# Performance work log

Measured on AMD Instinct MI355X. Metric: run time of the kernel, lower is better.

Reference implementation:

```python
import jax, jax.numpy as jnp
import numpy as np

B = 16384  # batch
D = 1024   # input_size (== hidden_size, required by the original code)
H = 1024   # hidden_size


def setup_inputs() -> dict:
    key = jax.random.key(0)
    ks = jax.random.split(key, 20)
    s = 0.02
    inp = {
        "x": jax.random.normal(ks[0], (B, D), dtype=jnp.float32),
        "h": jax.random.normal(ks[1], (B, H), dtype=jnp.float32),
        "c_prev": jax.random.normal(ks[2], (B, H), dtype=jnp.float32),
    }
    names = ["i_x", "f_x", "c_x", "o_x", "i_h", "f_h", "c_h", "o_h"]
    for n, name in enumerate(names):
        in_dim = D if name.endswith("_x") else H
        inp["W" + name] = jax.random.normal(ks[3 + 2 * n], (H, in_dim), dtype=jnp.float32) * s
        inp["b" + name] = jax.random.normal(ks[4 + 2 * n], (H,), dtype=jnp.float32) * s
    return inp


def reference(x, h, c_prev,
              Wi_x, bi_x, Wf_x, bf_x, Wc_x, bc_x, Wo_x, bo_x,
              Wi_h, bi_h, Wf_h, bf_h, Wc_h, bc_h, Wo_h, bo_h):
    # NOTE: the original module applies NO sigmoid to the gates; i, f, o are raw affine sums.
    i = x @ Wi_x.T + bi_x + h @ Wi_h.T + bi_h
    f = x @ Wf_x.T + bf_x + h @ Wf_h.T + bf_h
    g = jnp.tanh(x @ Wc_x.T + bc_x + h @ Wc_h.T + bc_h)
    o = x @ Wo_x.T + bo_x + h @ Wo_h.T + bo_h
    c_next = g * i + c_prev * f
    h_next = o * jnp.tanh(c_next)
    return (h_next, c_next)
```

## Files before the change

### kernel.cpp

```cpp
#include <hip/hip_runtime.h>
#include <hip/hip_bf16.h>


#define MROWS 16384
#define NCOLS 1024
#define KTOT  2048

typedef __attribute__((ext_vector_type(8))) short bf16x8;
typedef __attribute__((ext_vector_type(4))) float f32x4;
typedef unsigned int u32;
typedef unsigned short u16;

__device__ __forceinline__ u16 f2bf(float f) {
  union { float f; u32 u; } v; v.f = f;
  u32 r = v.u + 0x7fffu + ((v.u >> 16) & 1u);
  return (u16)(r >> 16);
}

__device__ __forceinline__ bf16x8 pack8(float4 lo, float4 hi) {
  bf16x8 v;
  v[0] = (short)f2bf(lo.x); v[1] = (short)f2bf(lo.y);
  v[2] = (short)f2bf(lo.z); v[3] = (short)f2bf(lo.w);
  v[4] = (short)f2bf(hi.x); v[5] = (short)f2bf(hi.y);
  v[6] = (short)f2bf(hi.z); v[7] = (short)f2bf(hi.w);
  return v;
}

__device__ __forceinline__ float tanh_fast(float x) {
  float e = __expf(2.0f * x);
  return 1.0f - 2.0f / (e + 1.0f);
}

typedef __attribute__((address_space(1))) const u32 gas_u32;
typedef __attribute__((address_space(3))) u32 las_u32;

__device__ __forceinline__ void gl_lds16(const void* g, void* l) {
  __builtin_amdgcn_global_load_lds((gas_u32*)g, (las_u32*)l, 16, 0, 0);
}

__global__ void __launch_bounds__(256) convA(const float* __restrict__ x,
                                             const float* __restrict__ h,
                                             u16* __restrict__ A) {
  u32 t = blockIdx.x * 256u + threadIdx.x;
  #pragma unroll
  for (int i = 0; i < 4; ++i) {
    u32 chunk = t + (u32)i * 1048576u;
    u32 row = chunk >> 8;
    u32 cpos = (chunk & 255u) * 8u;
    const float* src = (cpos < 1024u) ? (x + (size_t)row * 1024 + cpos)
                                      : (h + (size_t)row * 1024 + (cpos - 1024u));
    float4 lo = *(const float4*)src;
    float4 hi = *(const float4*)(src + 4);
    *(bf16x8*)(A + (size_t)chunk * 8) = pack8(lo, hi);
  }
}

__global__ void __launch_bounds__(256) convW(const float* __restrict__ wix, const float* __restrict__ wfx,
                                             const float* __restrict__ wcx, const float* __restrict__ wox,
                                             const float* __restrict__ wih, const float* __restrict__ wfh,
                                             const float* __restrict__ wch, const float* __restrict__ woh,
                                             u16* __restrict__ W) {
  u32 t = blockIdx.x * 256u + threadIdx.x;
  const float* WX[4] = {wix, wfx, wcx, wox};
  const float* WH[4] = {wih, wfh, wch, woh};
  #pragma unroll
  for (int g = 0; g < 4; ++g) {
    u32 c3 = t;
    u32 n = c3 >> 8;
    u32 cpos = (c3 & 255u) * 8u;
    const float* src = (cpos < 1024u) ? (WX[g] + (size_t)n * 1024 + cpos)
                                      : (WH[g] + (size_t)n * 1024 + (cpos - 1024u));
    float4 lo = *(const float4*)src;
    float4 hi = *(const float4*)(src + 4);
    *(bf16x8*)(W + (size_t)g * 2097152 + (size_t)c3 * 8) = pack8(lo, hi);
  }
}

__global__ void __launch_bounds__(512) lstm_gemm2(
    const u16* __restrict__ Abf, const u16* __restrict__ Wbf,
    const float* __restrict__ bix, const float* __restrict__ bfx,
    const float* __restrict__ bcx, const float* __restrict__ box_,
    const float* __restrict__ bih, const float* __restrict__ bfh,
    const float* __restrict__ bch, const float* __restrict__ boh,
    const float* __restrict__ cprev, float* __restrict__ out) {
  __shared__ alignas(16) u16 sA[2 * 16384];
  __shared__ alignas(16) u16 sB[2 * 16384];

  const u32 tid = threadIdx.x;
  const u32 lane = tid & 63u, wid = tid >> 6;
  const u32 wr = wid >> 1, wc = wid & 1u;
  const u32 l15 = lane & 15u, l4 = lane >> 4;

  const u32 bid = blockIdx.x;
  const u32 sid = (bid & 7u) * 128u + (bid >> 3);
  const u32 bm = sid >> 4, bn = sid & 15u;

  const u16* gAp[4];
  const u16* gBp[4];
  #pragma unroll
  for (int j = 0; j < 4; ++j) {
    u32 chunk = wid * 256u + (u32)j * 64u + lane;
    u32 row = chunk >> 3, k8 = chunk & 7u;
    u32 col16 = k8 ^ (row & 7u);
    gAp[j] = Abf + (size_t)(bm * 256u + row) * KTOT + col16 * 8u;
    u32 Wrow = (row >> 6) * 1024u + bn * 64u + (row & 63u);
    gBp[j] = Wbf + (size_t)Wrow * KTOT + col16 * 8u;
  }

#define STAGE(ktile, dbuf) do { \
    _Pragma("unroll") \
    for (int j = 0; j < 4; ++j) { \
      u32 dst = (dbuf) * 16384u + (wid * 256u + (u32)j * 64u) * 8u; \
      gl_lds16(gAp[j] + (u32)(ktile) * 64u, sA + dst); \
      gl_lds16(gBp[j] + (u32)(ktile) * 64u, sB + dst); \
    } \
  } while (0)

  const char* cA = (const char*)sA;
  const char* cB = (const char*)sB;
  const u32 kb[2] = { l4 * 16u, 64u + l4 * 16u };

  f32x4 acc[4][4][2];
  #pragma unroll
  for (int mf = 0; mf < 4; ++mf)
    #pragma unroll
    for (int g = 0; g < 4; ++g)
      #pragma unroll
      for (int nf = 0; nf < 2; ++nf)
        acc[mf][g][nf] = (f32x4){0.f, 0.f, 0.f, 0.f};

  STAGE(0, 0);
  __syncthreads();

  #pragma unroll 2
  for (int kt = 0; kt < 32; ++kt) {
    const u32 d = (u32)kt & 1u, dn = d ^ 1u;
    const u32 dO = d * 32768u;

    if (kt < 31) STAGE(kt + 1, dn);
    __builtin_amdgcn_sched_barrier(0);

    bf16x8 af[4][2];
    #pragma unroll
    for (int mf = 0; mf < 4; ++mf) {
      u32 mrow = wr * 64u + (u32)mf * 16u + l15;
      u32 rb = dO + mrow * 128u;
      u32 sw = (mrow & 7u) << 4;
      af[mf][0] = *(const bf16x8*)(cA + rb + (kb[0] ^ sw));
      af[mf][1] = *(const bf16x8*)(cA + rb + (kb[1] ^ sw));
    }

    __builtin_amdgcn_s_setprio(1);
    #pragma unroll
    for (int s = 0; s < 2; ++s)
      #pragma unroll
      for (int g = 0; g < 4; ++g)
        #pragma unroll
        for (int nf = 0; nf < 2; ++nf) {
          u32 brow = (u32)g * 64u + wc * 32u + (u32)nf * 16u + l15;
          u32 off = dO + brow * 128u + (kb[s] ^ ((brow & 7u) << 4));
          bf16x8 bfr = *(const bf16x8*)(cB + off);
          #pragma unroll
          for (int mf = 0; mf < 4; ++mf)
            acc[mf][g][nf] = __builtin_amdgcn_mfma_f32_16x16x32_bf16(af[mf][s], bfr, acc[mf][g][nf], 0, 0, 0);
        }
    __builtin_amdgcn_s_setprio(0);

    __syncthreads();
  }
#undef STAGE

  #pragma unroll
  for (int nf = 0; nf < 2; ++nf) {
    u32 col = bn * 64u + wc * 32u + (u32)nf * 16u + l15;
    float bi = bix[col] + bih[col];
    float bff = bfx[col] + bfh[col];
    float bc = bcx[col] + bch[col];
    float bo = box_[col] + boh[col];
    #pragma unroll
    for (int mf = 0; mf < 4; ++mf) {
      u32 row0 = bm * 256u + wr * 64u + (u32)mf * 16u + l4 * 4u;
      #pragma unroll
      for (int r = 0; r < 4; ++r) {
        size_t idx = (size_t)(row0 + (u32)r) * 1024 + col;
        float iv = acc[mf][0][nf][r] + bi;
        float fv = acc[mf][1][nf][r] + bff;
        float gv = tanh_fast(acc[mf][2][nf][r] + bc);
        float ov = acc[mf][3][nf][r] + bo;
        float cp = cprev[idx];
        float cn = gv * iv + cp * fv;
        out[idx] = ov * tanh_fast(cn);
        out[(size_t)16777216 + idx] = cn;
      }
    }
  }
}

__global__ void __launch_bounds__(256, 2) lstm_gemm_fb(
    const float* __restrict__ x, const float* __restrict__ h,
    const float* __restrict__ wix, const float* __restrict__ wfx,
    const float* __restrict__ wcx, const float* __restrict__ wox,
    const float* __restrict__ wih, const float* __restrict__ wfh,
    const float* __restrict__ wch, const float* __restrict__ woh,
    const float* __restrict__ bix, const float* __restrict__ bfx,
    const float* __restrict__ bcx, const float* __restrict__ box_,
    const float* __restrict__ bih, const float* __restrict__ bfh,
    const float* __restrict__ bch, const float* __restrict__ boh,
    const float* __restrict__ cprev, float* __restrict__ out) {
  __shared__ alignas(16) u16 sA[128 * 64];
  __shared__ alignas(16) u16 sB[4 * 64 * 64];
  const u32 tid = threadIdx.x;
  const u32 lane = tid & 63u;
  const u32 wid = tid >> 6;
  const u32 wr = wid >> 1, wc = wid & 1u;
  const u32 bidx = blockIdx.x;
  const u32 bm = bidx >> 4, bn = bidx & 15u;
  f32x4 acc[4][4][2];
  #pragma unroll
  for (int g = 0; g < 4; ++g)
    #pragma unroll
    for (int m = 0; m < 4; ++m)
      #pragma unroll
      for (int n = 0; n < 2; ++n)
        acc[g][m][n] = (f32x4){0.f, 0.f, 0.f, 0.f};
  const u32 l15 = lane & 15u, l4 = lane >> 4;
  for (int kt = 0; kt < KTOT / 64; ++kt) {
    const u32 k0 = (u32)kt * 64u;
    if (kt) __syncthreads();
    #pragma unroll
    for (int c = 0; c < 4; ++c) {
      u32 chunk = tid + (u32)c * 256u;
      u32 row = chunk >> 3;
      u32 cp = (chunk & 7u) * 8u;
      u32 gk = k0 + cp;
      const float* src = (gk < 1024u) ? (x + (size_t)(bm * 128u + row) * 1024 + gk)
                                      : (h + (size_t)(bm * 128u + row) * 1024 + (gk - 1024u));
      float4 lo = *(const float4*)src;
      float4 hi = *(const float4*)(src + 4);
      u32 dst = row * 128u + ((cp * 2u) ^ ((row & 7u) << 4));
      *(bf16x8*)((char*)sA + dst) = pack8(lo, hi);
    }
    #pragma unroll
    for (int g = 0; g < 4; ++g) {
      const float* Wxg = (g == 0) ? wix : (g == 1) ? wfx : (g == 2) ? wcx : wox;
      const float* Whg = (g == 0) ? wih : (g == 1) ? wfh : (g == 2) ? wch : woh;
      #pragma unroll
      for (int cc = 0; cc < 2; ++cc) {
        u32 c3 = tid + (u32)cc * 256u;
        u32 row = c3 >> 3;
        u32 cp = (c3 & 7u) * 8u;
        u32 gk = k0 + cp;
        const float* src = (gk < 1024u) ? (Wxg + (size_t)(bn * 64u + row) * 1024 + gk)
                                        : (Whg + (size_t)(bn * 64u + row) * 1024 + (gk - 1024u));
        float4 lo = *(const float4*)src;
        float4 hi = *(const float4*)(src + 4);
        u32 dst = (u32)g * 8192u + row * 128u + ((cp * 2u) ^ ((row & 7u) << 4));
        *(bf16x8*)((char*)sB + dst) = pack8(lo, hi);
      }
    }
    __syncthreads();
    #pragma unroll
    for (int s = 0; s < 2; ++s) {
      bf16x8 af[4];
      #pragma unroll
      for (int m = 0; m < 4; ++m) {
        u32 mrow = wr * 64u + (u32)m * 16u + l15;
        u32 off = mrow * 128u + (((u32)s * 64u + l4 * 16u) ^ ((mrow & 7u) << 4));
        af[m] = *(const bf16x8*)((const char*)sA + off);
      }
      #pragma unroll
      for (int g = 0; g < 4; ++g) {
        #pragma unroll
        for (int nf = 0; nf < 2; ++nf) {
          u32 nrow = wc * 32u + (u32)nf * 16u + l15;
          u32 off = (u32)g * 8192u + nrow * 128u +
                    (((u32)s * 64u + l4 * 16u) ^ ((nrow & 7u) << 4));
          bf16x8 bfr = *(const bf16x8*)((const char*)sB + off);
          #pragma unroll
          for (int m = 0; m < 4; ++m)
            acc[g][m][nf] = __builtin_amdgcn_mfma_f32_16x16x32_bf16(af[m], bfr, acc[g][m][nf], 0, 0, 0);
        }
      }
    }
  }
  #pragma unroll
  for (int nf = 0; nf < 2; ++nf) {
    u32 col = bn * 64u + wc * 32u + (u32)nf * 16u + l15;
    float bi = bix[col] + bih[col];
    float bff = bfx[col] + bfh[col];
    float bc = bcx[col] + bch[col];
    float bo = box_[col] + boh[col];
    #pragma unroll
    for (int m = 0; m < 4; ++m) {
      u32 row0 = bm * 128u + wr * 64u + (u32)m * 16u + l4 * 4u;
      #pragma unroll
      for (int r = 0; r < 4; ++r) {
        size_t idx = (size_t)(row0 + (u32)r) * 1024 + col;
        float iv = acc[0][m][nf][r] + bi;
        float fv = acc[1][m][nf][r] + bff;
        float gv = tanh_fast(acc[2][m][nf][r] + bc);
        float ov = acc[3][m][nf][r] + bo;
        float cp = cprev[idx];
        float cn = gv * iv + cp * fv;
        out[idx] = ov * tanh_fast(cn);
        out[(size_t)16777216 + idx] = cn;
      }
    }
  }
}

extern "C" void kernel_launch(void* const* d_in, const int* in_sizes, int n_in,
                              void* d_out, int out_size, void* d_ws, size_t ws_size,
                              hipStream_t stream) {
  const float* x = (const float*)d_in[0];
  const float* h = (const float*)d_in[1];
  const float* cprev = (const float*)d_in[2];
  const float* wix = (const float*)d_in[3];  const float* bix = (const float*)d_in[4];
  const float* wfx = (const float*)d_in[5];  const float* bfx = (const float*)d_in[6];
  const float* wcx = (const float*)d_in[7];  const float* bcx = (const float*)d_in[8];
  const float* wox = (const float*)d_in[9];  const float* box_ = (const float*)d_in[10];
  const float* wih = (const float*)d_in[11]; const float* bih = (const float*)d_in[12];
  const float* wfh = (const float*)d_in[13]; const float* bfh = (const float*)d_in[14];
  const float* wch = (const float*)d_in[15]; const float* bch = (const float*)d_in[16];
  const float* woh = (const float*)d_in[17]; const float* boh = (const float*)d_in[18];
  float* out = (float*)d_out;

  const size_t needA = (size_t)MROWS * KTOT * 2;
  const size_t needW = (size_t)4 * NCOLS * KTOT * 2;

  if (ws_size >= needA + needW) {
    u16* Abf = (u16*)d_ws;
    u16* Wbf = (u16*)((char*)d_ws + needA);
    convA<<<dim3(4096), dim3(256), 0, stream>>>(x, h, Abf);
    convW<<<dim3(1024), dim3(256), 0, stream>>>(wix, wfx, wcx, wox, wih, wfh, wch, woh, Wbf);
    lstm_gemm2<<<dim3(1024), dim3(512), 0, stream>>>(
        Abf, Wbf, bix, bfx, bcx, box_, bih, bfh, bch, boh, cprev, out);
  } else {
    lstm_gemm_fb<<<dim3(2048), dim3(256), 0, stream>>>(
        x, h, wix, wfx, wcx, wox, wih, wfh, wch, woh,
        bix, bfx, bcx, box_, bih, bfh, bch, boh, cprev, out);
  }
}
```

Measured before the change: 357.2 us.

## Shrink GEMM block tile to 128x256 with K-tile 32 for two blocks per CU

Replaces the 512-thread, 256x256-output block with 256-thread blocks covering 128 rows by 256 gate-columns, and halves the K tile from 64 to 32. LDS use per block falls from 128KB to 48KB, so two blocks can be resident per CU and the grid doubles to 2048 blocks. The swizzle is adapted to 4 chunks per row, and the XCD block remapping is adjusted for the larger grid. In exchange, the smaller tile lowers operand reuse, so more LDS and global traffic is needed per FLOP, and there are twice as many K iterations, each with its own barrier.

```diff
diff --git a/kernel.cpp b/kernel.cpp
--- a/kernel.cpp
+++ b/kernel.cpp
@@ -76,94 +76,92 @@
   }
 }
 
-__global__ void __launch_bounds__(512) lstm_gemm2(
+__global__ void __launch_bounds__(256, 2) lstm_gemm3(
     const u16* __restrict__ Abf, const u16* __restrict__ Wbf,
     const float* __restrict__ bix, const float* __restrict__ bfx,
     const float* __restrict__ bcx, const float* __restrict__ box_,
     const float* __restrict__ bih, const float* __restrict__ bfh,
     const float* __restrict__ bch, const float* __restrict__ boh,
     const float* __restrict__ cprev, float* __restrict__ out) {
-  __shared__ alignas(16) u16 sA[2 * 16384];
-  __shared__ alignas(16) u16 sB[2 * 16384];
+  __shared__ alignas(16) u16 sA[2 * 4096];
+  __shared__ alignas(16) u16 sB[2 * 8192];
 
   const u32 tid = threadIdx.x;
-  const u32 lane = tid & 63u, wid = tid >> 6;
+  const u32 lane = tid & 63u;
+  const u32 wid = tid >> 6;
   const u32 wr = wid >> 1, wc = wid & 1u;
   const u32 l15 = lane & 15u, l4 = lane >> 4;
 
-  const u32 bid = blockIdx.x;
-  const u32 sid = (bid & 7u) * 128u + (bid >> 3);
+  const u32 bidx = blockIdx.x;
+  const u32 sid = (bidx & 7u) * 256u + (bidx >> 3);
   const u32 bm = sid >> 4, bn = sid & 15u;
 
-  const u16* gAp[4];
+  const u16* gAp[2];
   const u16* gBp[4];
   #pragma unroll
+  for (int j = 0; j < 2; ++j) {
+    u32 c = (wid * 2u + (u32)j) * 64u + lane;
+    u32 row = c >> 2, k8 = c & 3u;
+    u32 col16 = k8 ^ (row & 3u);
+    gAp[j] = Abf + (size_t)(bm * 128u + row) * KTOT + col16 * 8u;
+  }
+  #pragma unroll
   for (int j = 0; j < 4; ++j) {
-    u32 chunk = wid * 256u + (u32)j * 64u + lane;
-    u32 row = chunk >> 3, k8 = chunk & 7u;
-    u32 col16 = k8 ^ (row & 7u);
-    gAp[j] = Abf + (size_t)(bm * 256u + row) * KTOT + col16 * 8u;
-    u32 Wrow = (row >> 6) * 1024u + bn * 64u + (row & 63u);
-    gBp[j] = Wbf + (size_t)Wrow * KTOT + col16 * 8u;
+    u32 c = (wid * 4u + (u32)j) * 64u + lane;
+    u32 brow = c >> 2, k8 = c & 3u;
+    u32 Wrow = (brow >> 6) * 1024u + bn * 64u + (brow & 63u);
+    gBp[j] = Wbf + (size_t)Wrow * KTOT + (k8 ^ (brow & 3u)) * 8u;
   }
 
 #define STAGE(ktile, dbuf) do { \
     _Pragma("unroll") \
-    for (int j = 0; j < 4; ++j) { \
-      u32 dst = (dbuf) * 16384u + (wid * 256u + (u32)j * 64u) * 8u; \
-      gl_lds16(gAp[j] + (u32)(ktile) * 64u, sA + dst); \
-      gl_lds16(gBp[j] + (u32)(ktile) * 64u, sB + dst); \
-    } \
+    for (int j = 0; j < 2; ++j) \
+      gl_lds16(gAp[j] + (u32)(ktile) * 32u, sA + (dbuf) * 4096u + (wid * 2u + (u32)j) * 512u); \
+    _Pragma("unroll") \
+    for (int j = 0; j < 4; ++j) \
+      gl_lds16(gBp[j] + (u32)(ktile) * 32u, sB + (dbuf) * 8192u + (wid * 4u + (u32)j) * 512u); \
   } while (0)
 
   const char* cA = (const char*)sA;
   const char* cB = (const char*)sB;
-  const u32 kb[2] = { l4 * 16u, 64u + l4 * 16u };
 
   f32x4 acc[4][4][2];
   #pragma unroll
-  for (int mf = 0; mf < 4; ++mf)
-    #pragma unroll
-    for (int g = 0; g < 4; ++g)
-      #pragma unroll
-      for (int nf = 0; nf < 2; ++nf)
-        acc[mf][g][nf] = (f32x4){0.f, 0.f, 0.f, 0.f};
+  for (int g = 0; g < 4; ++g)
+    #pragma unroll
+    for (int m = 0; m < 4; ++m)
+      #pragma unroll
+      for (int n = 0; n < 2; ++n)
+        acc[g][m][n] = (f32x4){0.f, 0.f, 0.f, 0.f};
 
   STAGE(0, 0);
   __syncthreads();
 
   #pragma unroll 2
-  for (int kt = 0; kt < 32; ++kt) {
+  for (int kt = 0; kt < 64; ++kt) {
     const u32 d = (u32)kt & 1u, dn = d ^ 1u;
-    const u32 dO = d * 32768u;
-
-    if (kt < 31) STAGE(kt + 1, dn);
+
+    if (kt < 63) STAGE(kt + 1, dn);
     __builtin_amdgcn_sched_barrier(0);
 
-    bf16x8 af[4][2];
+    bf16x8 af[4];
     #pragma unroll
     for (int mf = 0; mf < 4; ++mf) {
       u32 mrow = wr * 64u + (u32)mf * 16u + l15;
-      u32 rb = dO + mrow * 128u;
-      u32 sw = (mrow & 7u) << 4;
-      af[mf][0] = *(const bf16x8*)(cA + rb + (kb[0] ^ sw));
-      af[mf][1] = *(const bf16x8*)(cA + rb + (kb[1] ^ sw));
+      af[mf] = *(const bf16x8*)(cA + d * 8192u + mrow * 64u + ((l4 ^ (mrow & 3u)) << 4));
     }
 
     __builtin_amdgcn_s_setprio(1);
     #pragma unroll
-    for (int s = 0; s < 2; ++s)
-      #pragma unroll
-      for (int g = 0; g < 4; ++g)
+    for (int g = 0; g < 4; ++g)
+      #pragma unroll
+      for (int nf = 0; nf < 2; ++nf) {
+        u32 brow = (u32)g * 64u + wc * 32u + (u32)nf * 16u + l15;
+        bf16x8 bfr = *(const bf16x8*)(cB + d * 16384u + brow * 64u + ((l4 ^ (brow & 3u)) << 4));
         #pragma unroll
-        for (int nf = 0; nf < 2; ++nf) {
-          u32 brow = (u32)g * 64u + wc * 32u + (u32)nf * 16u + l15;
-          u32 off = dO + brow * 128u + (kb[s] ^ ((brow & 7u) << 4));
-          bf16x8 bfr = *(const bf16x8*)(cB + off);
-          #pragma unroll
-          for (int mf = 0; mf < 4; ++mf)
-            acc[mf][g][nf] = __builtin_amdgcn_mfma_f32_16x16x32_bf16(af[mf][s], bfr, acc[mf][g][nf], 0, 0, 0);
-        }
+        for (int m = 0; m < 4; ++m)
+          acc[g][m][nf] = __builtin_amdgcn_mfma_f32_16x16x32_bf16(af[m], bfr, acc[g][m][nf], 0, 0, 0);
+      }
     __builtin_amdgcn_s_setprio(0);
 
     __syncthreads();
@@ -178,15 +176,15 @@
     float bc = bcx[col] + bch[col];
     float bo = box_[col] + boh[col];
     #pragma unroll
-    for (int mf = 0; mf < 4; ++mf) {
-      u32 row0 = bm * 256u + wr * 64u + (u32)mf * 16u + l4 * 4u;
+    for (int m = 0; m < 4; ++m) {
+      u32 row0 = bm * 128u + wr * 64u + (u32)m * 16u + l4 * 4u;
       #pragma unroll
       for (int r = 0; r < 4; ++r) {
         size_t idx = (size_t)(row0 + (u32)r) * 1024 + col;
-        float iv = acc[mf][0][nf][r] + bi;
-        float fv = acc[mf][1][nf][r] + bff;
-        float gv = tanh_fast(acc[mf][2][nf][r] + bc);
-        float ov = acc[mf][3][nf][r] + bo;
+        float iv = acc[0][m][nf][r] + bi;
+        float fv = acc[1][m][nf][r] + bff;
+        float gv = tanh_fast(acc[2][m][nf][r] + bc);
+        float ov = acc[3][m][nf][r] + bo;
         float cp = cprev[idx];
         float cn = gv * iv + cp * fv;
         out[idx] = ov * tanh_fast(cn);
@@ -333,7 +331,7 @@
     u16* Wbf = (u16*)((char*)d_ws + needA);
     convA<<<dim3(4096), dim3(256), 0, stream>>>(x, h, Abf);
     convW<<<dim3(1024), dim3(256), 0, stream>>>(wix, wfx, wcx, wox, wih, wfh, wch, woh, Wbf);
-    lstm_gemm2<<<dim3(1024), dim3(512), 0, stream>>>(
+    lstm_gemm3<<<dim3(2048), dim3(256), 0, stream>>>(
         Abf, Wbf, bix, bfx, bcx, box_, bih, bfh, bch, boh, cprev, out);
   } else {
     lstm_gemm_fb<<<dim3(2048), dim3(256), 0, stream>>>(
```

After: 368.3 us. 1.03x slower.
